# Kernel optimization log

Hardware: AMD Instinct MI355X
Metric: run time of the kernel (lower is better)

The kernel has to match this reference:

```python
import math
import jax, jax.numpy as jnp
import numpy as np
from math import comb

MV_DIM = 32   # 2**5, Cl(5) multivector dimension
N_HEADS = 8
HIDDEN = N_HEADS * MV_DIM
B, L = 2, 2048


def _reverse_grade_signs(n=5):
    # sign of blade reversal: (-1)^{k(k-1)/2} per grade k, C(n,k) blades per grade
    signs = []
    for k in range(n + 1):
        s = (-1.0) ** ((k * (k - 1)) // 2)
        signs += [s] * comb(n, k)
    return jnp.asarray(np.array(signs, dtype=np.float32))


def setup_inputs() -> dict:
    key = jax.random.key(0)
    ks = jax.random.split(key, 7)
    x = jax.random.normal(ks[0], (B, L, MV_DIM), dtype=jnp.float32)
    mask = jax.random.randint(ks[1], (B, L, L), 0, 2).astype(bool)
    w_scale = 1.0 / math.sqrt(MV_DIM)
    Wq = jax.random.normal(ks[2], (HIDDEN, MV_DIM), dtype=jnp.float32) * w_scale
    Wk = jax.random.normal(ks[3], (HIDDEN, MV_DIM), dtype=jnp.float32) * w_scale
    Wv = jax.random.normal(ks[4], (HIDDEN, MV_DIM), dtype=jnp.float32) * w_scale
    Wo = jax.random.normal(ks[5], (MV_DIM, HIDDEN), dtype=jnp.float32) * (1.0 / math.sqrt(HIDDEN))
    # Cayley table for the geometric product: gp[n,k] = sum_ij a[n,i] b[n,j] C[i,j,k]
    cayley = jax.random.normal(ks[6], (MV_DIM, MV_DIM, MV_DIM), dtype=jnp.float32) * 0.1
    grade_signs = _reverse_grade_signs(5)
    return {"x": x, "mask": mask, "Wq": Wq, "Wk": Wk, "Wv": Wv, "Wo": Wo,
            "cayley": cayley, "grade_signs": grade_signs}


def reference(x, mask, Wq, Wk, Wv, Wo, cayley, grade_signs):
    Bx, Lx, D = x.shape           # D == MV_DIM == head_dim
    H = N_HEADS
    scale = 1.0 / math.sqrt(D)

    def proj(W):  # [B,L,D] -> [B,H,L,D]
        return (x @ W.T).reshape(Bx, Lx, H, D).transpose(0, 2, 1, 3)

    Q = proj(Wq)
    K = proj(Wk)
    V = proj(Wv)

    # grade-sign reweighted keys
    attn = jnp.einsum('bhld,bhmd->bhlm', Q, K * grade_signs) * scale
    m = mask[:, None, :, :]                       # [B,1,L,L] broadcast over heads
    row_valid = jnp.any(m, axis=-1, keepdims=True)  # [B,1,L,1]
    attn = jnp.where(m, attn, jnp.float32(-1e9))
    attn = jnp.where(row_valid, attn, jnp.float32(0.0))
    w = jax.nn.softmax(attn, axis=-1)

    V_agg = jnp.einsum('bhlm,bhmd->bhld', w, V)

    # Clifford geometric products via Cayley table
    gp_qv = jnp.einsum('bhli,bhlj,ijk->bhlk', Q, V_agg, cayley)
    gp_qk = jnp.einsum('bhli,bhlj,ijk->bhlk', Q, K, cayley)
    out = gp_qv + V_agg + 0.25 * gp_qk
    out = out * row_valid.astype(out.dtype)

    out = out.transpose(0, 2, 1, 3).reshape(Bx, Lx, H * D)
    return out @ Wo.T
```

## Files before the change

### kernel.cpp

```cpp
#include <hip/hip_runtime.h>
#include <hip/hip_bf16.h>
#include <stdint.h>
#include <stddef.h>

#define LL 2048

typedef __attribute__((ext_vector_type(8))) short short8;
typedef __attribute__((ext_vector_type(4))) float f32x4;
typedef unsigned short ushort_t;
typedef unsigned int uint_t;

#define VAOFF   1048576u
#define QS16OFF 2097152u
#define KS16OFF 2621440u
#define KG16OFF 3145728u
#define VT16OFF 3670016u
#define RVOFF   4194304u
#define MBOFF   4198400u
#define C2TOFF  4460544u

__device__ __forceinline__ ushort_t f2bf(float f) {
    unsigned int u = __float_as_uint(f);
    u += 0x7FFFu + ((u >> 16) & 1u);
    return (ushort_t)(u >> 16);
}
__device__ __forceinline__ float bf2f(ushort_t s) {
    return __uint_as_float(((unsigned int)s) << 16);
}
__device__ __forceinline__ uint_t pkbf(float a, float b) {
    __hip_bfloat162 h = __float22bfloat162_rn(float2{a, b});
    return *(uint_t*)&h;
}
__device__ __forceinline__ uint_t cvtpk(float a, float b) {
    uint_t r;
    asm("v_cvt_pk_bf16_f32 %0, %1, %2" : "=v"(r) : "v"(a), "v"(b));
    return r;
}
__device__ __forceinline__ float fexp2(float x) {
#if __has_builtin(__builtin_amdgcn_exp2f)
    return __builtin_amdgcn_exp2f(x);
#else
    float r; asm("v_exp_f32 %0, %1" : "=v"(r) : "v"(x)); return r;
#endif
}

__global__ __launch_bounds__(256) void prep_kernel(
        const uint_t* __restrict__ mraw, uint_t* __restrict__ mb,
        const float* __restrict__ x,
        const float* __restrict__ Wq, const float* __restrict__ Wk,
        const float* __restrict__ Wv, const float* __restrict__ gs,
        const float* __restrict__ cayley, float* __restrict__ ws) {
    __shared__ float smem[8192];
    const int t = threadIdx.x;

    if (blockIdx.x < 1024) {
        int* sI = (int*)smem;
        int* sF = ((int*)smem) + 1;
        if (t == 0) { *sI = 1; *sF = 1; }
        __syncthreads();
        const size_t blk = blockIdx.x;
        const uint4* p8 = (const uint4*)(mraw + blk * 2048 + t * 8);
        const uint4 a = p8[0], c = p8[1];
        const uint_t d8[8] = {a.x, a.y, a.z, a.w, c.x, c.y, c.z, c.w};
        int oi = 1, of = 1;
#pragma unroll
        for (int i = 0; i < 8; ++i) {
            if (d8[i] > 1u) oi = 0;
            if (d8[i] != 0u && d8[i] != 0x3F800000u) of = 0;
        }
        if (!oi) atomicAnd(sI, 0);
        if (!of) atomicAnd(sF, 0);
        __syncthreads();
        const int mtype = *sI ? 1 : (*sF ? 2 : 0);
        uint_t w = 0;
        if (mtype == 0) {
#pragma unroll
            for (int i = 0; i < 8; ++i) {
#pragma unroll
                for (int by = 0; by < 4; ++by)
                    w |= (((d8[i] >> (8 * by)) & 0xFFu) ? 1u : 0u) << (i * 4 + by);
            }
        } else {
            const uint4* pi = (const uint4*)(mraw + blk * 8192 + (size_t)t * 32);
#pragma unroll
            for (int i = 0; i < 8; ++i) {
                const uint4 d = pi[i];
                if (mtype == 1) {
                    w |= (d.x << (i * 4)) | (d.y << (i * 4 + 1)) |
                         (d.z << (i * 4 + 2)) | (d.w << (i * 4 + 3));
                } else {
                    w |= ((d.x ? 1u : 0u) << (i * 4)) | ((d.y ? 1u : 0u) << (i * 4 + 1)) |
                         ((d.z ? 1u : 0u) << (i * 4 + 2)) | ((d.w ? 1u : 0u) << (i * 4 + 3));
                }
            }
        }
        const uint_t W = (uint_t)(blk * 256 + t);
        const uint_t w0 = W & 63u;
        mb[(W & ~63u) | (((w0 & 3u) << 4) | (w0 >> 2))] = w;
    } else if (blockIdx.x < 1536) {
        ushort_t* Qs16 = (ushort_t*)(ws + QS16OFF);
        ushort_t* Ks16 = (ushort_t*)(ws + KS16OFF);
        ushort_t* Kg16 = (ushort_t*)(ws + KG16OFF);
        ushort_t* Vt   = (ushort_t*)(ws + VT16OFF);
        float* sX = smem;
        const int pid0 = (blockIdx.x - 1024) * 8;
        if (t < 64) ((float4*)sX)[t] = ((const float4*)(x + (size_t)pid0 * 32))[t];
        float wq[32], wk[32], wv[32];
        const float4* wqp = (const float4*)(Wq + t * 32);
        const float4* wkp = (const float4*)(Wk + t * 32);
        const float4* wvp = (const float4*)(Wv + t * 32);
#pragma unroll
        for (int d4 = 0; d4 < 8; ++d4) {
            float4 a = wqp[d4]; wq[4*d4]=a.x; wq[4*d4+1]=a.y; wq[4*d4+2]=a.z; wq[4*d4+3]=a.w;
            float4 b = wkp[d4]; wk[4*d4]=b.x; wk[4*d4+1]=b.y; wk[4*d4+2]=b.z; wk[4*d4+3]=b.w;
            float4 c = wvp[d4]; wv[4*d4]=c.x; wv[4*d4+1]=c.y; wv[4*d4+2]=c.z; wv[4*d4+3]=c.w;
        }
        const float sgn = gs[t & 31];
        const float qscale = 0.17677669529663687f * 1.4426950408889634f;
        const int h = t >> 5, dd = t & 31;
        const int b0 = pid0 >> 11, l0 = pid0 & 2047;
        __syncthreads();
        ushort4 vt4[2];
        for (int r = 0; r < 8; ++r) {
            const int pid = pid0 + r;
            const int b = pid >> 11, l = pid & 2047;
            float q = 0.f, k = 0.f, v = 0.f;
#pragma unroll
            for (int d = 0; d < 32; ++d) {
                const float xv = sX[r * 32 + d];
                q += xv * wq[d]; k += xv * wk[d]; v += xv * wv[d];
            }
            const size_t o = ((size_t)((b * 8 + h) * 2048 + l)) * 32 + dd;
            Qs16[o] = f2bf(q * qscale);
            Ks16[o] = f2bf(k * sgn);
            Kg16[o] = f2bf(k);
            ((ushort_t*)&vt4[r >> 2])[r & 3] = f2bf(v);
        }
        ushort_t* vtrow = Vt + ((size_t)((b0 * 8 + h) * 32 + dd)) * 2048;
#pragma unroll
        for (int g4 = 0; g4 < 2; ++g4) {
            const int lg = l0 + g4 * 4;
            const int lloc = lg & 63;
            const int g = lloc >> 5, tt = (lloc >> 4) & 1, q4 = (lloc >> 2) & 3;
            const int pc = (lg & ~63) + g * 32 + q4 * 8 + tt * 4;
            *(ushort4*)(vtrow + pc) = vt4[g4];
        }
    } else {
        float* sC = smem;
        ushort_t* C2t = (ushort_t*)(ws + C2TOFF);
        const int ij0 = (blockIdx.x - 1536) * 256;
#pragma unroll
        for (int i = 0; i < 8; ++i)
            ((float4*)sC)[t + i * 256] = ((const float4*)(cayley + (size_t)ij0 * 32))[t + i * 256];
        __syncthreads();
        const int k = t & 31, jc = t >> 5;
        uint_t pk[16];
#pragma unroll
        for (int j2 = 0; j2 < 16; ++j2) {
            pk[j2] = pkbf(sC[(jc * 32 + 2 * j2) * 32 + k], sC[(jc * 32 + 2 * j2 + 1) * 32 + k]);
        }
        uint_t* dst = (uint_t*)(C2t + (size_t)k * 1024 + ij0 + jc * 32);
#pragma unroll
        for (int j2 = 0; j2 < 16; ++j2) dst[j2] = pk[j2];
    }
}

__global__ __launch_bounds__(256, 4) void attn_kernel(
        const uint_t* __restrict__ mb, float* __restrict__ ws) {
    const ushort_t* Qs = (const ushort_t*)(ws + QS16OFF);
    const ushort_t* Ks = (const ushort_t*)(ws + KS16OFF);
    const ushort_t* Vt = (const ushort_t*)(ws + VT16OFF);
    float* Va = ws + VAOFF;
    float* Rv = ws + RVOFF;

    const int bid = blockIdx.x;
    const int bh = ((bid & 7) << 1) | ((bid >> 9) & 1);
    const int q0 = ((bid >> 3) & 63) * 32;
    const int b = bh >> 3;
    const int t = threadIdx.x;
    const int ks = t >> 6, lane = t & 63;
    const int quad = lane >> 4, l15 = lane & 15;

    __shared__ float accb[3][2][64][8];
    __shared__ float psL[4][32];

    const ushort_t* qbase = Qs + ((size_t)(bh * 2048 + q0 + l15)) * 32 + quad * 8;
    const short8 qfA = *(const short8*)(qbase);
    const short8 qfB = *(const short8*)(qbase + 16 * 32);

    const ushort_t* ka_p = Ks + (size_t)bh * 65536 + (ks * 32 + l15) * 32 + quad * 8;
    const ushort_t* v0_p = Vt + (size_t)bh * 65536 + (size_t)l15 * 2048 + ks * 32 + quad * 8;
    const uint_t* m_pA = mb + ((size_t)b * 2048 + q0 + l15) * 64 + ks * 16;
    const uint_t* m_pB = m_pA + 16 * 64;

    f32x4 accA0 = {0.f, 0.f, 0.f, 0.f};
    f32x4 accA1 = {0.f, 0.f, 0.f, 0.f};
    f32x4 accA2 = {0.f, 0.f, 0.f, 0.f};
    f32x4 accB0 = {0.f, 0.f, 0.f, 0.f};
    f32x4 accB1 = {0.f, 0.f, 0.f, 0.f};
    f32x4 accB2 = {0.f, 0.f, 0.f, 0.f};
    const int bp0 = quad * 4, bp1 = 16 + quad * 4;

    union { uint_t u[4]; short8 s; } ONES;
    {
        const uint_t ov = (l15 == 0) ? 0x3F803F80u : 0u;
        ONES.u[0] = ov; ONES.u[1] = ov; ONES.u[2] = ov; ONES.u[3] = ov;
    }

#pragma unroll 2
    for (int kt = 0; kt < 16; ++kt) {
        const short8 ka = *(const short8*)(ka_p + kt * 4096);
        const short8 kb = *(const short8*)(ka_p + kt * 4096 + 512);
        const short8 v0 = *(const short8*)(v0_p + kt * 128);
        const short8 v1 = *(const short8*)(v0_p + 16 * 2048 + kt * 128);
        const uint_t mwA = m_pA[kt];
        const uint_t mwB = m_pB[kt];

        const f32x4 z = {0.f, 0.f, 0.f, 0.f};
        f32x4 s0 = __builtin_amdgcn_mfma_f32_16x16x32_bf16(ka, qfA, z, 0, 0, 0);
        f32x4 s1 = __builtin_amdgcn_mfma_f32_16x16x32_bf16(kb, qfA, z, 0, 0, 0);
        f32x4 s2 = __builtin_amdgcn_mfma_f32_16x16x32_bf16(ka, qfB, z, 0, 0, 0);
        f32x4 s3 = __builtin_amdgcn_mfma_f32_16x16x32_bf16(kb, qfB, z, 0, 0, 0);

        float pA0[4], pA1[4], pB0[4], pB1[4];
#pragma unroll
        for (int r = 0; r < 4; ++r) {
            pA0[r] = ((mwA >> (bp0 + r)) & 1u) ? fexp2(s0[r]) : 0.f;
            pA1[r] = ((mwA >> (bp1 + r)) & 1u) ? fexp2(s1[r]) : 0.f;
            pB0[r] = ((mwB >> (bp0 + r)) & 1u) ? fexp2(s2[r]) : 0.f;
            pB1[r] = ((mwB >> (bp1 + r)) & 1u) ? fexp2(s3[r]) : 0.f;
        }
        union { uint_t u[4]; short8 s; } PA, PB;
        PA.u[0] = cvtpk(pA0[0], pA0[1]); PA.u[1] = cvtpk(pA0[2], pA0[3]);
        PA.u[2] = cvtpk(pA1[0], pA1[1]); PA.u[3] = cvtpk(pA1[2], pA1[3]);
        PB.u[0] = cvtpk(pB0[0], pB0[1]); PB.u[1] = cvtpk(pB0[2], pB0[3]);
        PB.u[2] = cvtpk(pB1[0], pB1[1]); PB.u[3] = cvtpk(pB1[2], pB1[3]);

        accA0 = __builtin_amdgcn_mfma_f32_16x16x32_bf16(PA.s, v0, accA0, 0, 0, 0);
        accA1 = __builtin_amdgcn_mfma_f32_16x16x32_bf16(PA.s, v1, accA1, 0, 0, 0);
        accA2 = __builtin_amdgcn_mfma_f32_16x16x32_bf16(PA.s, ONES.s, accA2, 0, 0, 0);
        accB0 = __builtin_amdgcn_mfma_f32_16x16x32_bf16(PB.s, v0, accB0, 0, 0, 0);
        accB1 = __builtin_amdgcn_mfma_f32_16x16x32_bf16(PB.s, v1, accB1, 0, 0, 0);
        accB2 = __builtin_amdgcn_mfma_f32_16x16x32_bf16(PB.s, ONES.s, accB2, 0, 0, 0);
    }

    if (l15 == 0) {
#pragma unroll
        for (int r = 0; r < 4; ++r) {
            psL[ks][quad * 4 + r] = accA2[r];
            psL[ks][16 + quad * 4 + r] = accB2[r];
        }
    }
    if (ks != 0) {
#pragma unroll
        for (int i = 0; i < 4; ++i) {
            accb[ks - 1][0][lane][i] = accA0[i];
            accb[ks - 1][0][lane][4 + i] = accA1[i];
            accb[ks - 1][1][lane][i] = accB0[i];
            accb[ks - 1][1][lane][4 + i] = accB1[i];
        }
    }
    __syncthreads();
    if (ks == 0) {
#pragma unroll
        for (int p = 0; p < 3; ++p) {
#pragma unroll
            for (int i = 0; i < 4; ++i) {
                accA0[i] += accb[p][0][lane][i];
                accA1[i] += accb[p][0][lane][4 + i];
                accB0[i] += accb[p][1][lane][i];
                accB1[i] += accb[p][1][lane][4 + i];
            }
        }
#pragma unroll
        for (int r = 0; r < 4; ++r) {
            const int rowA = quad * 4 + r;
            const int rowB = 16 + quad * 4 + r;
            const float totA = psL[0][rowA] + psL[1][rowA] + psL[2][rowA] + psL[3][rowA];
            const float totB = psL[0][rowB] + psL[1][rowB] + psL[2][rowB] + psL[3][rowB];
            const float invA = (totA > 0.f) ? 1.0f / totA : 0.f;
            const float invB = (totB > 0.f) ? 1.0f / totB : 0.f;
            const size_t oA = ((size_t)(bh * 2048 + q0 + rowA)) * 32;
            const size_t oB = ((size_t)(bh * 2048 + q0 + rowB)) * 32;
            Va[oA + l15] = accA0[r] * invA;
            Va[oA + 16 + l15] = accA1[r] * invA;
            Va[oB + l15] = accB0[r] * invB;
            Va[oB + 16 + l15] = accB1[r] * invB;
            if ((bh & 7) == 0 && l15 == 0) {
                Rv[(size_t)b * 2048 + q0 + rowA] = (totA > 0.f) ? 1.0f : 0.f;
                Rv[(size_t)b * 2048 + q0 + rowB] = (totB > 0.f) ? 1.0f : 0.f;
            }
        }
    }
}

__global__ __launch_bounds__(256) void gp_kernel(
        const float* __restrict__ ws, const float* __restrict__ Wo,
        float* __restrict__ out) {
    const float* Va = ws + VAOFF;
    const ushort_t* Qs = (const ushort_t*)(ws + QS16OFF);
    const ushort_t* Kg = (const ushort_t*)(ws + KG16OFF);
    const ushort_t* C2t = (const ushort_t*)(ws + C2TOFF);
    const float* Rv = ws + RVOFF;
    __shared__ ushort_t sC[32 * 1040];
    __shared__ float sH[64 * 32];

    const int t = threadIdx.x;
    const int w = t >> 6, lane = t & 63;
    const int quad = lane >> 4, l15 = lane & 15;

#pragma unroll
    for (int j = 0; j < 16; ++j) {
        const int c = j * 256 + t;
        const int row = c >> 7, col = (c & 127) * 8;
        *(short8*)(&sC[row * 1040 + col]) = *(const short8*)(C2t + row * 1024 + col);
    }

    const int grow0 = blockIdx.x * 64 + w * 16 + l15;
    const int pos = grow0 >> 3, h = grow0 & 7;
    const int b = pos >> 11, l = pos & 2047;
    const size_t gb = ((size_t)((b * 8 + h) * 2048 + l)) * 32;

    float q[32];
#pragma unroll
    for (int j8 = 0; j8 < 4; ++j8) {
        const short8 qv = *(const short8*)(Qs + gb + j8 * 8);
#pragma unroll
        for (int i = 0; i < 8; ++i) q[j8 * 8 + i] = bf2f((ushort_t)qv[i]);
    }
    float u[8];
    {
        const short8 kv = *(const short8*)(Kg + gb + quad * 8);
        const float4 va0 = *(const float4*)(Va + gb + quad * 8);
        const float4 va1 = *(const float4*)(Va + gb + quad * 8 + 4);
        u[0] = va0.x + 0.25f * bf2f((ushort_t)kv[0]);
        u[1] = va0.y + 0.25f * bf2f((ushort_t)kv[1]);
        u[2] = va0.z + 0.25f * bf2f((ushort_t)kv[2]);
        u[3] = va0.w + 0.25f * bf2f((ushort_t)kv[3]);
        u[4] = va1.x + 0.25f * bf2f((ushort_t)kv[4]);
        u[5] = va1.y + 0.25f * bf2f((ushort_t)kv[5]);
        u[6] = va1.z + 0.25f * bf2f((ushort_t)kv[6]);
        u[7] = va1.w + 0.25f * bf2f((ushort_t)kv[7]);
    }
    __syncthreads();

    f32x4 a0 = {0.f, 0.f, 0.f, 0.f};
    f32x4 a1 = {0.f, 0.f, 0.f, 0.f};
    const ushort_t* b0p = sC + (size_t)l15 * 1040 + quad * 8;
    const ushort_t* b1p = sC + (size_t)(16 + l15) * 1040 + quad * 8;

#pragma unroll
    for (int kc = 0; kc < 32; ++kc) {
        const float qk = q[kc];
        union { uint_t u4[4]; short8 s; } F;
        F.u4[0] = cvtpk(qk * u[0], qk * u[1]);
        F.u4[1] = cvtpk(qk * u[2], qk * u[3]);
        F.u4[2] = cvtpk(qk * u[4], qk * u[5]);
        F.u4[3] = cvtpk(qk * u[6], qk * u[7]);
        const short8 bb0 = *(const short8*)(b0p + kc * 32);
        const short8 bb1 = *(const short8*)(b1p + kc * 32);
        a0 = __builtin_amdgcn_mfma_f32_16x16x32_bf16(F.s, bb0, a0, 0, 0, 0);
        a1 = __builtin_amdgcn_mfma_f32_16x16x32_bf16(F.s, bb1, a1, 0, 0, 0);
    }

    const float SQ32 = 5.656854249492381f * 0.69314718055994531f;
#pragma unroll
    for (int r = 0; r < 4; ++r) {
        const int grow = blockIdx.x * 64 + w * 16 + quad * 4 + r;
        const int pr = grow >> 3, hr = grow & 7;
        const int br = pr >> 11, lr = pr & 2047;
        const size_t vb = ((size_t)((br * 8 + hr) * 2048 + lr)) * 32;
        const float rv = Rv[pr];
        sH[(w * 16 + quad * 4 + r) * 32 + l15] = (a0[r] * SQ32 + Va[vb + l15]) * rv;
        sH[(w * 16 + quad * 4 + r) * 32 + 16 + l15] = (a1[r] * SQ32 + Va[vb + 16 + l15]) * rv;
    }
    __syncthreads();

    float4* sWo4 = (float4*)sC;
    {
        const float4* wog = (const float4*)Wo;
#pragma unroll
        for (int i = 0; i < 8; ++i) {
            const int f = t + i * 256;
            const int row = f >> 6, j4 = f & 63;
            sWo4[row * 64 + (j4 ^ (row & 7))] = wog[f];
        }
    }
    __syncthreads();

    const int pp = t >> 5, d2 = t & 31;
    const float* hp = sH + pp * 256;
    const float4* wrow = sWo4 + d2 * 64;
    const int rswz = d2 & 7;
    float o = 0.f;
#pragma unroll 8
    for (int j4 = 0; j4 < 64; ++j4) {
        const float4 wv = wrow[j4 ^ rswz];
        const float4 hv = *(const float4*)(hp + j4 * 4);
        o += wv.x * hv.x + wv.y * hv.y + wv.z * hv.z + wv.w * hv.w;
    }
    out[((size_t)blockIdx.x * 8 + pp) * 32 + d2] = o;
}

extern "C" void kernel_launch(void* const* d_in, const int* in_sizes, int n_in,
                              void* d_out, int out_size, void* d_ws, size_t ws_size,
                              hipStream_t stream) {
    const float* x      = (const float*)d_in[0];
    const void*  mask   = d_in[1];
    const float* Wq     = (const float*)d_in[2];
    const float* Wk     = (const float*)d_in[3];
    const float* Wv     = (const float*)d_in[4];
    const float* Wo     = (const float*)d_in[5];
    const float* cayley = (const float*)d_in[6];
    const float* gs     = (const float*)d_in[7];
    float* out = (float*)d_out;
    float* ws  = (float*)d_ws;
    uint_t* mb = (uint_t*)(ws + MBOFF);

    prep_kernel<<<dim3(1540), dim3(256), 0, stream>>>(
        (const uint_t*)mask, mb, x, Wq, Wk, Wv, gs, cayley, ws);
    attn_kernel<<<dim3(1024), dim3(256), 0, stream>>>(mb, ws);
    gp_kernel<<<dim3(512), dim3(256), 0, stream>>>(ws, Wo, out);
}
```

Baseline: 154.0 us.

## Fold grade signs into Q, mask exp via LUT, use wave vote for mask type

The grade-sign reweighting moves from a separate sign-multiplied K copy onto the Q fragment by flipping bf16 sign bits in the attention kernel. This lets the prep kernel skip writing the Ks16 buffer, and the attention kernel now reads the ungraded K. Per-element masked selects before exp are replaced by an unconditional exp2 followed by an AND with a 16-entry shared-memory mask lookup table. Mask-type detection switches from per-thread shared atomics to wave-level __all votes, at the cost of an extra __syncthreads and LDS lookups in the inner loop.

```diff
diff --git a/kernel.cpp b/kernel.cpp
--- a/kernel.cpp
+++ b/kernel.cpp
@@ -12,7 +12,6 @@
 
 #define VAOFF   1048576u
 #define QS16OFF 2097152u
-#define KS16OFF 2621440u
 #define KG16OFF 3145728u
 #define VT16OFF 3670016u
 #define RVOFF   4194304u
@@ -48,7 +47,7 @@
         const uint_t* __restrict__ mraw, uint_t* __restrict__ mb,
         const float* __restrict__ x,
         const float* __restrict__ Wq, const float* __restrict__ Wk,
-        const float* __restrict__ Wv, const float* __restrict__ gs,
+        const float* __restrict__ Wv,
         const float* __restrict__ cayley, float* __restrict__ ws) {
     __shared__ float smem[8192];
     const int t = threadIdx.x;
@@ -68,8 +67,11 @@
             if (d8[i] > 1u) oi = 0;
             if (d8[i] != 0u && d8[i] != 0x3F800000u) of = 0;
         }
-        if (!oi) atomicAnd(sI, 0);
-        if (!of) atomicAnd(sF, 0);
+        const int ai = __all(oi), af = __all(of);
+        if ((t & 63) == 0) {
+            if (!ai) *sI = 0;
+            if (!af) *sF = 0;
+        }
         __syncthreads();
         const int mtype = *sI ? 1 : (*sF ? 2 : 0);
         uint_t w = 0;
@@ -99,7 +101,6 @@
         mb[(W & ~63u) | (((w0 & 3u) << 4) | (w0 >> 2))] = w;
     } else if (blockIdx.x < 1536) {
         ushort_t* Qs16 = (ushort_t*)(ws + QS16OFF);
-        ushort_t* Ks16 = (ushort_t*)(ws + KS16OFF);
         ushort_t* Kg16 = (ushort_t*)(ws + KG16OFF);
         ushort_t* Vt   = (ushort_t*)(ws + VT16OFF);
         float* sX = smem;
@@ -115,7 +116,6 @@
             float4 b = wkp[d4]; wk[4*d4]=b.x; wk[4*d4+1]=b.y; wk[4*d4+2]=b.z; wk[4*d4+3]=b.w;
             float4 c = wvp[d4]; wv[4*d4]=c.x; wv[4*d4+1]=c.y; wv[4*d4+2]=c.z; wv[4*d4+3]=c.w;
         }
-        const float sgn = gs[t & 31];
         const float qscale = 0.17677669529663687f * 1.4426950408889634f;
         const int h = t >> 5, dd = t & 31;
         const int b0 = pid0 >> 11, l0 = pid0 & 2047;
@@ -132,7 +132,6 @@
             }
             const size_t o = ((size_t)((b * 8 + h) * 2048 + l)) * 32 + dd;
             Qs16[o] = f2bf(q * qscale);
-            Ks16[o] = f2bf(k * sgn);
             Kg16[o] = f2bf(k);
             ((ushort_t*)&vt4[r >> 2])[r & 3] = f2bf(v);
         }
@@ -166,9 +165,10 @@
 }
 
 __global__ __launch_bounds__(256, 4) void attn_kernel(
-        const uint_t* __restrict__ mb, float* __restrict__ ws) {
+        const uint_t* __restrict__ mb, float* __restrict__ ws,
+        const float* __restrict__ gs) {
     const ushort_t* Qs = (const ushort_t*)(ws + QS16OFF);
-    const ushort_t* Ks = (const ushort_t*)(ws + KS16OFF);
+    const ushort_t* Kg = (const ushort_t*)(ws + KG16OFF);
     const ushort_t* Vt = (const ushort_t*)(ws + VT16OFF);
     float* Va = ws + VAOFF;
     float* Rv = ws + RVOFF;
@@ -183,12 +183,27 @@
 
     __shared__ float accb[3][2][64][8];
     __shared__ float psL[4][32];
+    __shared__ uint2 mlut[16];
+
+    if (t < 16) {
+        const uint_t lo = ((t & 1) ? 0xFFFFu : 0u) | ((t & 2) ? 0xFFFF0000u : 0u);
+        const uint_t hi = ((t & 4) ? 0xFFFFu : 0u) | ((t & 8) ? 0xFFFF0000u : 0u);
+        mlut[t] = uint2{lo, hi};
+    }
 
     const ushort_t* qbase = Qs + ((size_t)(bh * 2048 + q0 + l15)) * 32 + quad * 8;
-    const short8 qfA = *(const short8*)(qbase);
-    const short8 qfB = *(const short8*)(qbase + 16 * 32);
-
-    const ushort_t* ka_p = Ks + (size_t)bh * 65536 + (ks * 32 + l15) * 32 + quad * 8;
+    union { uint_t u[4]; short8 s; } QA, QB;
+    QA.s = *(const short8*)(qbase);
+    QB.s = *(const short8*)(qbase + 16 * 32);
+#pragma unroll
+    for (int i = 0; i < 4; ++i) {
+        const uint_t xlo = (gs[quad * 8 + 2 * i]     < 0.f) ? 0x00008000u : 0u;
+        const uint_t xhi = (gs[quad * 8 + 2 * i + 1] < 0.f) ? 0x80000000u : 0u;
+        const uint_t xo = xlo | xhi;
+        QA.u[i] ^= xo; QB.u[i] ^= xo;
+    }
+
+    const ushort_t* ka_p = Kg + (size_t)bh * 65536 + (ks * 32 + l15) * 32 + quad * 8;
     const ushort_t* v0_p = Vt + (size_t)bh * 65536 + (size_t)l15 * 2048 + ks * 32 + quad * 8;
     const uint_t* m_pA = mb + ((size_t)b * 2048 + q0 + l15) * 64 + ks * 16;
     const uint_t* m_pB = m_pA + 16 * 64;
@@ -206,6 +221,7 @@
         const uint_t ov = (l15 == 0) ? 0x3F803F80u : 0u;
         ONES.u[0] = ov; ONES.u[1] = ov; ONES.u[2] = ov; ONES.u[3] = ov;
     }
+    __syncthreads();
 
 #pragma unroll 2
     for (int kt = 0; kt < 16; ++kt) {
@@ -217,24 +233,33 @@
         const uint_t mwB = m_pB[kt];
 
         const f32x4 z = {0.f, 0.f, 0.f, 0.f};
-        f32x4 s0 = __builtin_amdgcn_mfma_f32_16x16x32_bf16(ka, qfA, z, 0, 0, 0);
-        f32x4 s1 = __builtin_amdgcn_mfma_f32_16x16x32_bf16(kb, qfA, z, 0, 0, 0);
-        f32x4 s2 = __builtin_amdgcn_mfma_f32_16x16x32_bf16(ka, qfB, z, 0, 0, 0);
-        f32x4 s3 = __builtin_amdgcn_mfma_f32_16x16x32_bf16(kb, qfB, z, 0, 0, 0);
-
-        float pA0[4], pA1[4], pB0[4], pB1[4];
+        f32x4 s0 = __builtin_amdgcn_mfma_f32_16x16x32_bf16(ka, QA.s, z, 0, 0, 0);
+        f32x4 s1 = __builtin_amdgcn_mfma_f32_16x16x32_bf16(kb, QA.s, z, 0, 0, 0);
+        f32x4 s2 = __builtin_amdgcn_mfma_f32_16x16x32_bf16(ka, QB.s, z, 0, 0, 0);
+        f32x4 s3 = __builtin_amdgcn_mfma_f32_16x16x32_bf16(kb, QB.s, z, 0, 0, 0);
+
+        const uint2 mA0 = mlut[(mwA >> bp0) & 15u];
+        const uint2 mA1 = mlut[(mwA >> bp1) & 15u];
+        const uint2 mB0 = mlut[(mwB >> bp0) & 15u];
+        const uint2 mB1 = mlut[(mwB >> bp1) & 15u];
+
+        float eA0[4], eA1[4], eB0[4], eB1[4];
 #pragma unroll
         for (int r = 0; r < 4; ++r) {
-            pA0[r] = ((mwA >> (bp0 + r)) & 1u) ? fexp2(s0[r]) : 0.f;
-            pA1[r] = ((mwA >> (bp1 + r)) & 1u) ? fexp2(s1[r]) : 0.f;
-            pB0[r] = ((mwB >> (bp0 + r)) & 1u) ? fexp2(s2[r]) : 0.f;
-            pB1[r] = ((mwB >> (bp1 + r)) & 1u) ? fexp2(s3[r]) : 0.f;
+            eA0[r] = fexp2(s0[r]);
+            eA1[r] = fexp2(s1[r]);
+            eB0[r] = fexp2(s2[r]);
+            eB1[r] = fexp2(s3[r]);
         }
         union { uint_t u[4]; short8 s; } PA, PB;
-        PA.u[0] = cvtpk(pA0[0], pA0[1]); PA.u[1] = cvtpk(pA0[2], pA0[3]);
-        PA.u[2] = cvtpk(pA1[0], pA1[1]); PA.u[3] = cvtpk(pA1[2], pA1[3]);
-        PB.u[0] = cvtpk(pB0[0], pB0[1]); PB.u[1] = cvtpk(pB0[2], pB0[3]);
-        PB.u[2] = cvtpk(pB1[0], pB1[1]); PB.u[3] = cvtpk(pB1[2], pB1[3]);
+        PA.u[0] = cvtpk(eA0[0], eA0[1]) & mA0.x;
+        PA.u[1] = cvtpk(eA0[2], eA0[3]) & mA0.y;
+        PA.u[2] = cvtpk(eA1[0], eA1[1]) & mA1.x;
+        PA.u[3] = cvtpk(eA1[2], eA1[3]) & mA1.y;
+        PB.u[0] = cvtpk(eB0[0], eB0[1]) & mB0.x;
+        PB.u[1] = cvtpk(eB0[2], eB0[3]) & mB0.y;
+        PB.u[2] = cvtpk(eB1[0], eB1[1]) & mB1.x;
+        PB.u[3] = cvtpk(eB1[2], eB1[3]) & mB1.y;
 
         accA0 = __builtin_amdgcn_mfma_f32_16x16x32_bf16(PA.s, v0, accA0, 0, 0, 0);
         accA1 = __builtin_amdgcn_mfma_f32_16x16x32_bf16(PA.s, v1, accA1, 0, 0, 0);
@@ -418,7 +443,7 @@
     uint_t* mb = (uint_t*)(ws + MBOFF);
 
     prep_kernel<<<dim3(1540), dim3(256), 0, stream>>>(
-        (const uint_t*)mask, mb, x, Wq, Wk, Wv, gs, cayley, ws);
-    attn_kernel<<<dim3(1024), dim3(256), 0, stream>>>(mb, ws);
+        (const uint_t*)mask, mb, x, Wq, Wk, Wv, cayley, ws);
+    attn_kernel<<<dim3(1024), dim3(256), 0, stream>>>(mb, ws, gs);
     gp_kernel<<<dim3(512), dim3(256), 0, stream>>>(ws, Wo, out);
 }
```

Measured after the change: 152.9 us, median of 2. Within noise of the previous version (-0.8%).
